# Performance work log

Measured on AMD Instinct MI355X. Metric: run time of the kernel, lower is better.

## Reference

```python
import jax, jax.numpy as jnp
import numpy as np

H, K, D, M = 16, 64, 1024, 4096
S, B = 2048, 4
EPS = 1e-5


def _ln(x, g, b):
    mu = jnp.mean(x, axis=-1, keepdims=True)
    var = jnp.var(x, axis=-1, keepdims=True)
    return (x - mu) / jnp.sqrt(var + EPS) * g + b


def setup_inputs() -> dict:
    key = jax.random.key(0)
    ks = jax.random.split(key, 8)
    std = 0.02
    x = jax.random.normal(ks[0], (S, B, D), jnp.float32)
    mask = jnp.zeros((S, S), jnp.float32)  # additive attention mask, broadcasts over (H*B, S, S)
    wq = jax.random.normal(ks[1], (H * K, D), jnp.float32) * std
    wk = jax.random.normal(ks[2], (H * K, D), jnp.float32) * std
    wv = jax.random.normal(ks[3], (H * K, D), jnp.float32) * std
    wc = jax.random.normal(ks[4], (D, H * K), jnp.float32) * std
    w1_w = jax.random.normal(ks[5], (M, D), jnp.float32) * std
    w1_b = jnp.zeros((M,), jnp.float32)
    w2_w = jax.random.normal(ks[6], (D, M), jnp.float32) * std
    w2_b = jnp.zeros((D,), jnp.float32)
    ln1_g = jnp.ones((D,), jnp.float32)
    ln1_b = jnp.zeros((D,), jnp.float32)
    ln2_g = jnp.ones((D,), jnp.float32)
    ln2_b = jnp.zeros((D,), jnp.float32)
    return dict(x=x, mask=mask, wq=wq, wk=wk, wv=wv, wc=wc, w1_w=w1_w, w1_b=w1_b,
                w2_w=w2_w, w2_b=w2_b, ln1_g=ln1_g, ln1_b=ln1_b, ln2_g=ln2_g, ln2_b=ln2_b)


def reference(x, mask, wq, wk, wv, wc, w1_w, w1_b, w2_w, w2_b, ln1_g, ln1_b, ln2_g, ln2_b):
    s, b, _ = x.shape
    q = (x @ wq.T).reshape(s, b, H, K)
    k = (x @ wk.T).reshape(s, b, H, K)
    v = (x @ wv.T).reshape(s, b, H, K)
    # scores: (B, H, S, S); mask (S, S) broadcasts over batch and heads as in torch
    scores = jnp.einsum('sbhk,tbhk->bhst', q, k) / jnp.sqrt(jnp.float32(K)) + mask
    alpha = jax.nn.softmax(scores, axis=-1)
    av = jnp.einsum('bhst,tbhk->sbhk', alpha, v).reshape(s, b, H * K)
    u = _ln(av @ wc.T + x, ln1_g, ln1_b)
    z = jax.nn.relu(u @ w1_w.T + w1_b) @ w2_w.T + w2_b
    return _ln(z + u, ln2_g, ln2_b)
```

## Files before the change

kernel.cpp:

```cpp
#include <hip/hip_runtime.h>
#include <math.h>

#define H_  16
#define K_  64
#define D_  1024
#define M_  4096
#define S_  2048
#define B_  4
#define N_  8192
#define HK_ 1024

typedef __attribute__((ext_vector_type(8))) short bfrag;
typedef __attribute__((ext_vector_type(4))) float f4;

typedef __attribute__((address_space(1))) const void g_void;
typedef __attribute__((address_space(3))) void s_void;

__device__ __forceinline__ float bf2f(unsigned short u){
  union { unsigned int i; float f; } x; x.i = ((unsigned int)u) << 16; return x.f;
}
__device__ __forceinline__ unsigned short f2bf(float f){
  unsigned int u = __float_as_uint(f);
  return (unsigned short)((u + 0x7fffu + ((u >> 16) & 1u)) >> 16);
}
__device__ __forceinline__ unsigned int pack2(float a, float b){
  return (unsigned int)f2bf(a) | ((unsigned int)f2bf(b) << 16);
}
__device__ __forceinline__ void gload16(const void* g, void* l){
  __builtin_amdgcn_global_load_lds((g_void*)g, (s_void*)l, 16, 0, 0);
}

__global__ __launch_bounds__(256) void castk(const float* __restrict__ in,
                                             unsigned short* __restrict__ out){
  int i = (blockIdx.x * 256 + threadIdx.x) * 4;
  float4 v = *(const float4*)(in + i);
  *(uint2*)(out + i) = make_uint2(pack2(v.x, v.y), pack2(v.z, v.w));
}

__global__ __launch_bounds__(256) void castw4(
    const float* __restrict__ a, const float* __restrict__ b,
    const float* __restrict__ c, const float* __restrict__ d,
    unsigned short* __restrict__ out){
  const int blk = blockIdx.x;
  const int seg = blk >> 10;
  const float* src = (seg == 0) ? a : (seg == 1) ? b : (seg == 2) ? c : d;
  const int rel = ((blk & 1023) * 256 + threadIdx.x) * 4;
  float4 v = *(const float4*)(src + rel);
  *(uint2*)(out + (size_t)seg * 1048576 + rel) = make_uint2(pack2(v.x, v.y), pack2(v.z, v.w));
}

__global__ __launch_bounds__(256) void mscale(const float* __restrict__ in,
                                              float* __restrict__ out){
  int i = (blockIdx.x * 256 + threadIdx.x) * 4;
  float4 v = *(const float4*)(in + i);
  const float c = 1.44269504f;
  v.x *= c; v.y *= c; v.z *= c; v.w *= c;
  *(float4*)(out + i) = v;
}

template<int EPI>
__global__ __launch_bounds__(256) void mgemm(
    const unsigned short* __restrict__ A, const unsigned short* __restrict__ W,
    const float* __restrict__ bias, const void* __restrict__ res,
    unsigned short* __restrict__ C, int Kdim, int Ncols)
{
  __shared__ unsigned short sA[3][4096];
  __shared__ unsigned short sB[3][4096];
  const int tid  = threadIdx.x;
  const int wave = tid >> 6, ln = tid & 63;
  const int lr   = ln & 15, quad = ln >> 4;
  const int m0   = blockIdx.y * 128, n0 = blockIdx.x * 128;
  const int wr   = (wave >> 1) * 64, wc = (wave & 1) * 64;
  const int segr = ln >> 2, segc = (ln & 3) * 8;
  const int sg   = wave * 2;

  const unsigned short* A0 = A + (size_t)(m0 + sg*16      + segr) * Kdim + segc;
  const unsigned short* A1 = A + (size_t)(m0 + sg*16 + 16 + segr) * Kdim + segc;
  const unsigned short* W0 = W + (size_t)(n0 + sg*16      + segr) * Kdim + segc;
  const unsigned short* W1 = W + (size_t)(n0 + sg*16 + 16 + segr) * Kdim + segc;

  const f4 zero = {0.f, 0.f, 0.f, 0.f};
  f4 acc[4][4];
  #pragma unroll
  for (int i=0;i<4;i++)
    #pragma unroll
    for (int j=0;j<4;j++) acc[i][j] = zero;

  auto stage = [&](int buf, int k0){
    gload16(A0 + k0, &sA[buf][sg*512]);
    gload16(A1 + k0, &sA[buf][sg*512 + 512]);
    gload16(W0 + k0, &sB[buf][sg*512]);
    gload16(W1 + k0, &sB[buf][sg*512 + 512]);
  };

  stage(0, 0);
  if (32 < Kdim) stage(1, 32);
  int cur = 0;

  for (int k0 = 0; k0 < Kdim; k0 += 32){
    if (k0 + 32 < Kdim) asm volatile("s_waitcnt vmcnt(4)" ::: "memory");
    else                asm volatile("s_waitcnt vmcnt(0)" ::: "memory");
    __builtin_amdgcn_s_barrier();
    int nxt = cur + 2; if (nxt >= 3) nxt -= 3;
    if (k0 + 64 < Kdim) stage(nxt, k0 + 64);

    bfrag af[4], bf[4];
    #pragma unroll
    for (int i=0;i<4;i++) af[i] = *(const bfrag*)&sA[cur][(wr + i*16 + lr)*32 + quad*8];
    #pragma unroll
    for (int j=0;j<4;j++) bf[j] = *(const bfrag*)&sB[cur][(wc + j*16 + lr)*32 + quad*8];
    #pragma unroll
    for (int i=0;i<4;i++)
      #pragma unroll
      for (int j=0;j<4;j++)
        acc[i][j] = __builtin_amdgcn_mfma_f32_16x16x32_bf16(af[i], bf[j], acc[i][j], 0, 0, 0);
    cur = (cur + 1 == 3) ? 0 : cur + 1;
  }

  #pragma unroll
  for (int i=0;i<4;i++){
    #pragma unroll
    for (int j=0;j<4;j++){
      #pragma unroll
      for (int r=0;r<4;r++){
        const int m = m0 + wr + i*16 + quad*4 + r;
        const int n = n0 + wc + j*16 + lr;
        float t = acc[i][j][r];
        if (EPI == 0){
          const int proj = n >> 10;
          const int s = m >> 2, b = m & 3, h = (n >> 6) & 15, kk = n & 63;
          C[(size_t)proj*8388608 + (((size_t)(b*16 + h)) * S_ + s) * 64 + kk] = f2bf(t);
        } else {
          const size_t off = (size_t)m * Ncols + n;
          if (EPI == 1) t += ((const float*)res)[off];
          if (EPI == 2) t = fmaxf(t + bias[n], 0.f);
          if (EPI == 3) t += bias[n] + bf2f(((const unsigned short*)res)[off]);
          C[off] = f2bf(t);
        }
      }
    }
  }
}

__global__ __launch_bounds__(256) void vtrans(const unsigned short* __restrict__ v,
                                              unsigned short* __restrict__ vT){
  const int tid = threadIdx.x;
  const int wave = tid >> 6, ln = tid & 63;
  const int bh = blockIdx.y;
  const int s  = blockIdx.x * 64 + ln;
  const int d0 = wave * 16;
  unsigned short tmp[16];
  const unsigned short* src = v + ((size_t)bh * S_ + s) * 64 + d0;
  *(uint4*)&tmp[0] = ((const uint4*)src)[0];
  *(uint4*)&tmp[8] = ((const uint4*)src)[1];
  unsigned short* dst = vT + (size_t)bh * 64 * S_ + s;
  #pragma unroll
  for (int e = 0; e < 16; e++)
    dst[(size_t)(d0 + e) * S_] = tmp[e];
}

__global__ __launch_bounds__(256) void fattn(
    const unsigned short* __restrict__ qg, const unsigned short* __restrict__ kg,
    const unsigned short* __restrict__ vT, const float* __restrict__ mb,
    unsigned short* __restrict__ av)
{
  __shared__ unsigned short Ks[2][4096];
  __shared__ unsigned short VTs[2][4096];
  __shared__ unsigned short Ps[4*32*72];
  const int tid  = threadIdx.x;
  const int wave = tid >> 6, ln = tid & 63;
  const int lr   = ln & 15, quad = ln >> 4;
  const int bh   = blockIdx.y;
  const int b    = bh >> 4, h = bh & 15;
  const int s0   = blockIdx.x * 128;
  const size_t base  = (size_t)bh * S_ * 64;
  const size_t tbase = (size_t)bh * 64 * S_;
  const int qw = s0 + wave*32;

  bfrag aq[2][2];
  #pragma unroll
  for (int qb=0;qb<2;qb++)
    #pragma unroll
    for (int hh=0;hh<2;hh++)
      aq[qb][hh] = *(const bfrag*)(qg + base + (size_t)(qw + qb*16 + lr)*64 + hh*32 + quad*8);

  const f4 zero = {0.f, 0.f, 0.f, 0.f};
  f4 acc[2][4];
  #pragma unroll
  for (int qb=0;qb<2;qb++)
    #pragma unroll
    for (int nb=0;nb<4;nb++) acc[qb][nb] = zero;
  float lsum[2][4];
  #pragma unroll
  for (int qb=0;qb<2;qb++)
    #pragma unroll
    for (int r=0;r<4;r++) lsum[qb][r] = 0.f;

  const int strow = wave*16 + (ln >> 3);
  const int scz   = ((ln & 7) ^ (ln >> 3)) * 8;
  const int rxor  = lr & 7;

  unsigned short* const psw = &Ps[wave*2304];

  const float* mrow[2][4];
  #pragma unroll
  for (int qb=0;qb<2;qb++)
    #pragma unroll
    for (int r=0;r<4;r++)
      mrow[qb][r] = mb + (size_t)(qw + qb*16 + quad*4 + r) * S_ + lr;

  auto stage = [&](int bufn, int t0n){
    unsigned short* kd = &Ks[bufn][(wave*16)*64];
    unsigned short* vd = &VTs[bufn][(wave*16)*64];
    gload16(kg + base  + (size_t)(t0n + strow    )*64 + scz, kd);
    gload16(kg + base  + (size_t)(t0n + strow + 8)*64 + scz, kd + 512);
    gload16(vT + tbase + (size_t)(strow    )*S_ + t0n + scz, vd);
    gload16(vT + tbase + (size_t)(strow + 8)*S_ + t0n + scz, vd + 512);
  };

  stage(0, 0);
  int cur = 0;

  for (int t0 = 0; t0 < S_; t0 += 64){
    __syncthreads();

    float mreg[2][4][4];
    #pragma unroll
    for (int qb=0;qb<2;qb++)
      #pragma unroll
      for (int r=0;r<4;r++)
        #pragma unroll
        for (int tb=0;tb<4;tb++)
          mreg[qb][r][tb] = mrow[qb][r][t0 + tb*16];

    if (t0 + 64 < S_) stage(cur ^ 1, t0 + 64);

    const unsigned short* Kc = Ks[cur];
    const unsigned short* Vc = VTs[cur];

    bfrag kf[4][2];
    #pragma unroll
    for (int tb=0;tb<4;tb++)
      #pragma unroll
      for (int hh=0;hh<2;hh++)
        kf[tb][hh] = *(const bfrag*)&Kc[(tb*16 + lr)*64 + (((hh*4 + quad) ^ rxor))*8];

    bfrag vf[4][2];
    #pragma unroll
    for (int nb=0;nb<4;nb++)
      #pragma unroll
      for (int hh=0;hh<2;hh++)
        vf[nb][hh] = *(const bfrag*)&Vc[(nb*16 + lr)*64 + (((hh*4 + quad) ^ rxor))*8];

    #pragma unroll
    for (int qb=0;qb<2;qb++){
      f4 sc[4];
      __builtin_amdgcn_s_setprio(1);
      #pragma unroll
      for (int tb=0;tb<4;tb++){
        f4 t = zero;
        t = __builtin_amdgcn_mfma_f32_16x16x32_bf16(aq[qb][0], kf[tb][0], t, 0, 0, 0);
        t = __builtin_amdgcn_mfma_f32_16x16x32_bf16(aq[qb][1], kf[tb][1], t, 0, 0, 0);
        sc[tb] = t;
      }
      __builtin_amdgcn_s_setprio(0);
      #pragma unroll
      for (int tb=0;tb<4;tb++){
        float p0 = __builtin_amdgcn_exp2f(fmaf(sc[tb][0], 0.18033688f, mreg[qb][0][tb]));
        float p1 = __builtin_amdgcn_exp2f(fmaf(sc[tb][1], 0.18033688f, mreg[qb][1][tb]));
        float p2 = __builtin_amdgcn_exp2f(fmaf(sc[tb][2], 0.18033688f, mreg[qb][2][tb]));
        float p3 = __builtin_amdgcn_exp2f(fmaf(sc[tb][3], 0.18033688f, mreg[qb][3][tb]));
        lsum[qb][0] += p0; lsum[qb][1] += p1;
        lsum[qb][2] += p2; lsum[qb][3] += p3;
        unsigned int pkA, pkB;
        asm("v_cvt_pk_bf16_f32 %0, %1, %2" : "=v"(pkA) : "v"(p0), "v"(p1));
        asm("v_cvt_pk_bf16_f32 %0, %1, %2" : "=v"(pkB) : "v"(p2), "v"(p3));
        unsigned short* pp = &psw[(qb*16 + quad*4)*72 + tb*16 + lr];
        pp[0]   = (unsigned short)pkA;
        pp[72]  = (unsigned short)(pkA >> 16);
        pp[144] = (unsigned short)pkB;
        pp[216] = (unsigned short)(pkB >> 16);
      }
    }

    __builtin_amdgcn_s_setprio(1);
    #pragma unroll
    for (int qb=0;qb<2;qb++){
      bfrag ap0 = *(const bfrag*)&psw[(qb*16 + lr)*72 + quad*8];
      bfrag ap1 = *(const bfrag*)&psw[(qb*16 + lr)*72 + 32 + quad*8];
      #pragma unroll
      for (int nb=0;nb<4;nb++){
        acc[qb][nb] = __builtin_amdgcn_mfma_f32_16x16x32_bf16(ap0, vf[nb][0], acc[qb][nb], 0, 0, 0);
        acc[qb][nb] = __builtin_amdgcn_mfma_f32_16x16x32_bf16(ap1, vf[nb][1], acc[qb][nb], 0, 0, 0);
      }
    }
    __builtin_amdgcn_s_setprio(0);
    cur ^= 1;
  }

  #pragma unroll
  for (int qb=0;qb<2;qb++)
    #pragma unroll
    for (int r=0;r<4;r++){
      float l = lsum[qb][r];
      l += __shfl_xor(l, 1);
      l += __shfl_xor(l, 2);
      l += __shfl_xor(l, 4);
      l += __shfl_xor(l, 8);
      const float inv = 1.f / l;
      const int qrow = qw + qb*16 + quad*4 + r;
      #pragma unroll
      for (int nb=0;nb<4;nb++)
        av[((size_t)qrow * B_ + b) * HK_ + h*64 + nb*16 + lr] = f2bf(acc[qb][nb][r] * inv);
    }
}

template<int OUTF32>
__global__ __launch_bounds__(256) void lnk(
    const unsigned short* __restrict__ pre, const float* __restrict__ g,
    const float* __restrict__ be, void* __restrict__ out)
{
  __shared__ float red[256];
  const int row = blockIdx.x;
  const int tid = threadIdx.x;
  const unsigned short* p = pre + (size_t)row * D_;
  uint2 raw = *(const uint2*)(p + tid*4);
  float x[4] = { bf2f(raw.x & 0xffffu), bf2f(raw.x >> 16),
                 bf2f(raw.y & 0xffffu), bf2f(raw.y >> 16) };
  red[tid] = x[0] + x[1] + x[2] + x[3];
  __syncthreads();
  for (int q = 128; q > 0; q >>= 1){
    if (tid < q) red[tid] += red[tid + q];
    __syncthreads();
  }
  const float mu = red[0] * (1.f / (float)D_);
  __syncthreads();
  float d0 = x[0]-mu, d1 = x[1]-mu, d2 = x[2]-mu, d3 = x[3]-mu;
  red[tid] = d0*d0 + d1*d1 + d2*d2 + d3*d3;
  __syncthreads();
  for (int q = 128; q > 0; q >>= 1){
    if (tid < q) red[tid] += red[tid + q];
    __syncthreads();
  }
  const float rstd = rsqrtf(red[0] * (1.f / (float)D_) + 1e-5f);
  const int c = tid * 4;
  #pragma unroll
  for (int j=0;j<4;j++){
    float y = (x[j] - mu) * rstd * g[c + j] + be[c + j];
    if (OUTF32) ((float*)out)[(size_t)row * D_ + c + j] = y;
    else ((unsigned short*)out)[(size_t)row * D_ + c + j] = f2bf(y);
  }
}

extern "C" void kernel_launch(void* const* d_in, const int* in_sizes, int n_in,
                              void* d_out, int out_size, void* d_ws, size_t ws_size,
                              hipStream_t stream) {
  const float* x    = (const float*)d_in[0];
  const float* mask = (const float*)d_in[1];
  const float* wq   = (const float*)d_in[2];
  const float* wk   = (const float*)d_in[3];
  const float* wv   = (const float*)d_in[4];
  const float* wc   = (const float*)d_in[5];
  const float* w1w  = (const float*)d_in[6];
  const float* w1b  = (const float*)d_in[7];
  const float* w2w  = (const float*)d_in[8];
  const float* w2b  = (const float*)d_in[9];
  const float* g1   = (const float*)d_in[10];
  const float* b1   = (const float*)d_in[11];
  const float* g2   = (const float*)d_in[12];
  const float* b2   = (const float*)d_in[13];

  unsigned short* ws = (unsigned short*)d_ws;
  unsigned short* xb   = ws + 0;
  unsigned short* wqb  = ws + 8388608;
  unsigned short* wkb  = ws + 9437184;
  unsigned short* wvb  = ws + 10485760;
  unsigned short* wcb  = ws + 11534336;
  unsigned short* q    = ws + 12582912;
  unsigned short* k    = ws + 20971520;
  unsigned short* v    = ws + 29360128;
  unsigned short* w1wb = ws + 37748736;
  unsigned short* w2wb = ws + 41943040;
  unsigned short* u    = ws + 46137344;
  unsigned short* z    = ws + 54525952;
  unsigned short* vT   = z;
  unsigned short* avb  = ws + 0;
  unsigned short* t1   = ws + 12582912;
  unsigned short* h1   = ws + 0;
  float*          mb   = (float*)(ws + 46137344);

  castk<<<8192, 256, 0, stream>>>(x,   xb);
  castw4<<<4096, 256, 0, stream>>>(wq, wk, wv, wc, wqb);
  castk<<<4096, 256, 0, stream>>>(w1w, w1wb);
  castk<<<4096, 256, 0, stream>>>(w2w, w2wb);
  mscale<<<4096, 256, 0, stream>>>(mask, mb);

  mgemm<0><<<dim3(24, 64), 256, 0, stream>>>(xb, wqb, nullptr, nullptr, q, D_, 3072);

  vtrans<<<dim3(S_/64, 64), 256, 0, stream>>>(v, vT);
  fattn<<<dim3(S_/128, B_*H_), 256, 0, stream>>>(q, k, vT, mb, avb);

  mgemm<1><<<dim3(8, 64), 256, 0, stream>>>(avb, wcb, nullptr, x, t1, HK_, D_);
  lnk<0><<<dim3(N_), 256, 0, stream>>>(t1, g1, b1, u);

  mgemm<2><<<dim3(32, 64), 256, 0, stream>>>(u, w1wb, w1b, nullptr, h1, D_, M_);

  mgemm<3><<<dim3(8, 64), 256, 0, stream>>>(h1, w2wb, w2b, u, z, M_, D_);
  lnk<1><<<dim3(N_), 256, 0, stream>>>(z, g2, b2, d_out);
}
```

Measured before the change: 590.9 us.

## Enlarge GEMM tile to 256x128 with 8 waves, XOR-swizzled LDS, K=64 steps

Restructures the bf16 MFMA GEMM to use 512-thread blocks computing 256x128 tiles with a K step of 64. LDS goes from triple to double buffering and uses an XOR swizzle to avoid bank conflicts, and s_setprio is raised around the MFMA burst. The aim is higher arithmetic intensity per tile and fewer barriers per unit of work. In exchange, each block uses more LDS and registers and the grid has fewer blocks, and the shallower prefetch pipeline may expose more load latency.

```diff
diff --git a/kernel.cpp b/kernel.cpp
--- a/kernel.cpp
+++ b/kernel.cpp
@@ -59,72 +59,80 @@
 }
 
 template<int EPI>
-__global__ __launch_bounds__(256) void mgemm(
+__global__ __launch_bounds__(512) void mgemm(
     const unsigned short* __restrict__ A, const unsigned short* __restrict__ W,
     const float* __restrict__ bias, const void* __restrict__ res,
     unsigned short* __restrict__ C, int Kdim, int Ncols)
 {
-  __shared__ unsigned short sA[3][4096];
-  __shared__ unsigned short sB[3][4096];
+  __shared__ unsigned short sA[2][16384];
+  __shared__ unsigned short sB[2][8192];
   const int tid  = threadIdx.x;
   const int wave = tid >> 6, ln = tid & 63;
   const int lr   = ln & 15, quad = ln >> 4;
-  const int m0   = blockIdx.y * 128, n0 = blockIdx.x * 128;
-  const int wr   = (wave >> 1) * 64, wc = (wave & 1) * 64;
-  const int segr = ln >> 2, segc = (ln & 3) * 8;
-  const int sg   = wave * 2;
-
-  const unsigned short* A0 = A + (size_t)(m0 + sg*16      + segr) * Kdim + segc;
-  const unsigned short* A1 = A + (size_t)(m0 + sg*16 + 16 + segr) * Kdim + segc;
-  const unsigned short* W0 = W + (size_t)(n0 + sg*16      + segr) * Kdim + segc;
-  const unsigned short* W1 = W + (size_t)(n0 + sg*16 + 16 + segr) * Kdim + segc;
+  const int m0   = blockIdx.y * 256, n0 = blockIdx.x * 128;
+  const int wr   = (wave >> 2) * 128;
+  const int wcn  = (wave & 3) * 32;
+  const int rxor = lr & 7;
+
+  const int srow = ln >> 3;
+  const int scz  = ((ln & 7) ^ srow) * 8;
+  const unsigned short* Asrc = A + (size_t)(m0 + wave*32 + srow) * Kdim + scz;
+  const unsigned short* Wsrc = W + (size_t)(n0 + wave*16 + srow) * Kdim + scz;
 
   const f4 zero = {0.f, 0.f, 0.f, 0.f};
-  f4 acc[4][4];
-  #pragma unroll
-  for (int i=0;i<4;i++)
-    #pragma unroll
-    for (int j=0;j<4;j++) acc[i][j] = zero;
+  f4 acc[8][2];
+  #pragma unroll
+  for (int i=0;i<8;i++){ acc[i][0] = zero; acc[i][1] = zero; }
 
   auto stage = [&](int buf, int k0){
-    gload16(A0 + k0, &sA[buf][sg*512]);
-    gload16(A1 + k0, &sA[buf][sg*512 + 512]);
-    gload16(W0 + k0, &sB[buf][sg*512]);
-    gload16(W1 + k0, &sB[buf][sg*512 + 512]);
+    unsigned short* ad = &sA[buf][(wave*32)*64];
+    #pragma unroll
+    for (int r8=0;r8<4;r8++)
+      gload16(Asrc + (size_t)r8*8*Kdim + k0, ad + r8*512);
+    unsigned short* bd = &sB[buf][(wave*16)*64];
+    gload16(Wsrc + k0, bd);
+    gload16(Wsrc + (size_t)8*Kdim + k0, bd + 512);
   };
 
   stage(0, 0);
-  if (32 < Kdim) stage(1, 32);
   int cur = 0;
 
-  for (int k0 = 0; k0 < Kdim; k0 += 32){
-    if (k0 + 32 < Kdim) asm volatile("s_waitcnt vmcnt(4)" ::: "memory");
-    else                asm volatile("s_waitcnt vmcnt(0)" ::: "memory");
-    __builtin_amdgcn_s_barrier();
-    int nxt = cur + 2; if (nxt >= 3) nxt -= 3;
-    if (k0 + 64 < Kdim) stage(nxt, k0 + 64);
-
-    bfrag af[4], bf[4];
-    #pragma unroll
-    for (int i=0;i<4;i++) af[i] = *(const bfrag*)&sA[cur][(wr + i*16 + lr)*32 + quad*8];
-    #pragma unroll
-    for (int j=0;j<4;j++) bf[j] = *(const bfrag*)&sB[cur][(wc + j*16 + lr)*32 + quad*8];
-    #pragma unroll
-    for (int i=0;i<4;i++)
-      #pragma unroll
-      for (int j=0;j<4;j++)
-        acc[i][j] = __builtin_amdgcn_mfma_f32_16x16x32_bf16(af[i], bf[j], acc[i][j], 0, 0, 0);
-    cur = (cur + 1 == 3) ? 0 : cur + 1;
-  }
-
-  #pragma unroll
-  for (int i=0;i<4;i++){
-    #pragma unroll
-    for (int j=0;j<4;j++){
+  for (int k0 = 0; k0 < Kdim; k0 += 64){
+    __syncthreads();
+    if (k0 + 64 < Kdim) stage(cur ^ 1, k0 + 64);
+
+    bfrag af[8][2], bf[2][2];
+    #pragma unroll
+    for (int i=0;i<8;i++)
+      #pragma unroll
+      for (int h=0;h<2;h++)
+        af[i][h] = *(const bfrag*)&sA[cur][(wr + i*16 + lr)*64 + ((h*4 + quad) ^ rxor)*8];
+    #pragma unroll
+    for (int j=0;j<2;j++)
+      #pragma unroll
+      for (int h=0;h<2;h++)
+        bf[j][h] = *(const bfrag*)&sB[cur][(wcn + j*16 + lr)*64 + ((h*4 + quad) ^ rxor)*8];
+
+    __builtin_amdgcn_s_setprio(1);
+    #pragma unroll
+    for (int i=0;i<8;i++)
+      #pragma unroll
+      for (int j=0;j<2;j++)
+        #pragma unroll
+        for (int h=0;h<2;h++)
+          acc[i][j] = __builtin_amdgcn_mfma_f32_16x16x32_bf16(af[i][h], bf[j][h], acc[i][j], 0, 0, 0);
+    __builtin_amdgcn_s_setprio(0);
+    cur ^= 1;
+  }
+
+  #pragma unroll
+  for (int i=0;i<8;i++){
+    #pragma unroll
+    for (int j=0;j<2;j++){
       #pragma unroll
       for (int r=0;r<4;r++){
         const int m = m0 + wr + i*16 + quad*4 + r;
-        const int n = n0 + wc + j*16 + lr;
+        const int n = n0 + wcn + j*16 + lr;
         float t = acc[i][j][r];
         if (EPI == 0){
           const int proj = n >> 10;
@@ -395,16 +403,16 @@
   castk<<<4096, 256, 0, stream>>>(w2w, w2wb);
   mscale<<<4096, 256, 0, stream>>>(mask, mb);
 
-  mgemm<0><<<dim3(24, 64), 256, 0, stream>>>(xb, wqb, nullptr, nullptr, q, D_, 3072);
+  mgemm<0><<<dim3(24, 32), 512, 0, stream>>>(xb, wqb, nullptr, nullptr, q, D_, 3072);
 
   vtrans<<<dim3(S_/64, 64), 256, 0, stream>>>(v, vT);
   fattn<<<dim3(S_/128, B_*H_), 256, 0, stream>>>(q, k, vT, mb, avb);
 
-  mgemm<1><<<dim3(8, 64), 256, 0, stream>>>(avb, wcb, nullptr, x, t1, HK_, D_);
+  mgemm<1><<<dim3(8, 32), 512, 0, stream>>>(avb, wcb, nullptr, x, t1, HK_, D_);
   lnk<0><<<dim3(N_), 256, 0, stream>>>(t1, g1, b1, u);
 
-  mgemm<2><<<dim3(32, 64), 256, 0, stream>>>(u, w1wb, w1b, nullptr, h1, D_, M_);
-
-  mgemm<3><<<dim3(8, 64), 256, 0, stream>>>(h1, w2wb, w2b, u, z, M_, D_);
+  mgemm<2><<<dim3(32, 32), 512, 0, stream>>>(u, w1wb, w1b, nullptr, h1, D_, M_);
+
+  mgemm<3><<<dim3(8, 32), 512, 0, stream>>>(h1, w2wb, w2b, u, z, M_, D_);
   lnk<1><<<dim3(N_), 256, 0, stream>>>(z, g2, b2, d_out);
 }
```

New measurement: 608.8 us. 1.03x slower.
